# Optimization experiments

Hardware: AMD Instinct MI355X
Metric: run time of the kernel (lower is better)

## Reference

```python
import jax, jax.numpy as jnp
import numpy as np

HID = 64
L = 3
RHO = 0.3
KMIN = 64
EPS = 1e-5


def conv1x1(x, w, b):
    # x: [B,C,H,W], w: [O,C], b: [O]
    return jnp.einsum('bchw,oc->bohw', x, w) + b[None, :, None, None]


def dwconv(x, w, pad, dil):
    # depthwise conv, w: [C,1,k,k], groups = C, no bias
    return jax.lax.conv_general_dilated(
        x, w, window_strides=(1, 1), padding=[(pad, pad), (pad, pad)],
        rhs_dilation=(dil, dil), feature_group_count=x.shape[1],
        dimension_numbers=('NCHW', 'OIHW', 'NCHW'))


def conv3x3(x, w, b):
    return jax.lax.conv_general_dilated(
        x, w, (1, 1), [(1, 1), (1, 1)],
        dimension_numbers=('NCHW', 'OIHW', 'NCHW')) + b[None, :, None, None]


def bn(x, g, b):
    # training-mode BatchNorm2d: batch statistics over (B,H,W) per channel
    mu = jnp.mean(x, axis=(0, 2, 3), keepdims=True)
    var = jnp.var(x, axis=(0, 2, 3), keepdims=True)
    return g[None, :, None, None] * (x - mu) * jax.lax.rsqrt(var + EPS) + b[None, :, None, None]


def setup_inputs() -> dict:
    key = jax.random.key(0)
    ks = jax.random.split(key, 40)
    B, C, H, W = 8, 1, 224, 224
    d = {}
    d['x'] = jax.random.normal(ks[0], (B, C, H, W), jnp.float32)
    # input_proj: 1x1 conv, out = 2*HID + L + 1 = 132
    d['w_in'] = jax.random.normal(ks[1], (2 * HID + L + 1, C), jnp.float32) * 0.5
    d['b_in'] = jnp.zeros((2 * HID + L + 1,), jnp.float32)
    for l in range(L):
        ksz = 2 * l + 3
        d[f'dw{l}'] = jax.random.normal(ks[2 + 4 * l], (HID, 1, ksz, ksz), jnp.float32) / ksz
        d[f'pw{l}_w'] = jax.random.normal(ks[3 + 4 * l], (HID, HID), jnp.float32) * (1.0 / np.sqrt(HID))
        d[f'pw{l}_b'] = jnp.zeros((HID,), jnp.float32)
        d[f'bn{l}_g'] = jnp.ones((HID,), jnp.float32)
        d[f'bn{l}_b'] = jnp.zeros((HID,), jnp.float32)
    d['imp_w1'] = jax.random.normal(ks[20], (HID // 4, HID), jnp.float32) * (1.0 / np.sqrt(HID))
    d['imp_b1'] = jnp.zeros((HID // 4,), jnp.float32)
    d['imp_w2'] = jax.random.normal(ks[21], (1, HID // 4, 3, 3), jnp.float32) * 0.1
    d['imp_b2'] = jnp.zeros((1,), jnp.float32)
    d['val_w'] = jax.random.normal(ks[22], (HID, HID), jnp.float32) * (1.0 / np.sqrt(HID))
    d['val_b'] = jnp.zeros((HID,), jnp.float32)
    d['out_w'] = jax.random.normal(ks[23], (HID, HID), jnp.float32) * (1.0 / np.sqrt(HID))
    d['out_b'] = jnp.zeros((HID,), jnp.float32)
    d['fin_w'] = jax.random.normal(ks[24], (HID, HID), jnp.float32) * (1.0 / np.sqrt(HID))
    d['fin_b'] = jnp.zeros((HID,), jnp.float32)
    return d


def reference(x, w_in, b_in,
              dw0, pw0_w, pw0_b, bn0_g, bn0_b,
              dw1, pw1_w, pw1_b, bn1_g, bn1_b,
              dw2, pw2_w, pw2_b, bn2_g, bn2_b,
              imp_w1, imp_b1, imp_w2, imp_b2,
              val_w, val_b, out_w, out_b, fin_w, fin_b):
    B, C, H, W = x.shape
    F_ = conv1x1(x, w_in, b_in)                       # [B, 2*HID+L+1, H, W]
    Q = F_[:, :HID]
    K = F_[:, HID:2 * HID]
    G = F_[:, 2 * HID:]                               # [B, L+1, H, W]
    # importance network: 1x1 conv -> ReLU -> 3x3 conv -> sigmoid
    imp = jax.nn.sigmoid(conv3x3(jax.nn.relu(conv1x1(K, imp_w1, imp_b1)), imp_w2, imp_b2))  # [B,1,H,W]
    # adaptive top-k sparsification: K = max(floor(rho*H*W), K_min)
    k = max(int(RHO * H * W), KMIN)
    mask_flat = imp.reshape(B, H * W)
    _, idx = jax.lax.top_k(mask_flat, k)              # [B, k]
    sparse = jnp.zeros_like(mask_flat).at[jnp.arange(B)[:, None], idx].set(1.0)
    K_cur = K * sparse.reshape(B, 1, H, W)
    # focal levels: kernel k_l = 2*l+3, dilation d_l = 2^l, pad = (k_l//2)*d_l
    levels = [(dw0, pw0_w, pw0_b, bn0_g, bn0_b, 1),
              (dw1, pw1_w, pw1_b, bn1_g, bn1_b, 2),
              (dw2, pw2_w, pw2_b, bn2_g, bn2_b, 4)]
    focal = []
    for dw, pw_w, pw_b, g, be, dil in levels:
        ksz = dw.shape[-1]
        pad = (ksz // 2) * dil
        K_cur = jax.nn.relu(bn(conv1x1(dwconv(K_cur, dw, pad, dil), pw_w, pw_b), g, be))
        focal.append(K_cur)
    Gn = jax.nn.softmax(G, axis=1)                    # softmax over L+1 gate channels
    K_agg = Gn[:, 0:1] * focal[0] + Gn[:, 1:2] * focal[1] + Gn[:, 2:3] * focal[2]
    K_global = jnp.mean(focal[-1], axis=(2, 3), keepdims=True)  # AdaptiveAvgPool2d(1), broadcast
    K_final = K_agg + Gn[:, -1:] * K_global
    V = conv1x1(K_final, val_w, val_b)
    QV = Q * V
    # output_proj Linear over channel dim (dropout is identity in eval)
    O = jnp.einsum('bchw,oc->bohw', QV, out_w) + out_b[None, :, None, None]
    # in_channels (1) != hidden_channels -> residual via final_conv on F[:, :HID] == Q
    x_proj = conv1x1(Q, fin_w, fin_b)
    return x_proj + O
```

## Files before the change

### kernel.cpp

```cpp
#include <hip/hip_runtime.h>

#define HDIM 224
#define WDIM 224
#define PPIX 50176
#define BATCH 8
#define NPIX 401408
#define KTOP 15052
#define NELEM 25690112
#define NBLK 6272
#define NBAND 14
#define NDWBLK 7168
#define NCHUNK 49

typedef __attribute__((ext_vector_type(8))) short bf8_t;
typedef __attribute__((ext_vector_type(4))) float f4_t;
typedef __attribute__((ext_vector_type(8))) unsigned short us8_t;
typedef __attribute__((ext_vector_type(4))) unsigned short us4_t;
#define MFMA_BF16 __builtin_amdgcn_mfma_f32_16x16x32_bf16

__device__ inline unsigned short f2bf(float f) {
    unsigned int u = __float_as_uint(f);
    return (unsigned short)((u + 0x7FFFu + ((u >> 16) & 1u)) >> 16);
}
__device__ inline float bf2f(unsigned short u) {
    return __uint_as_float(((unsigned int)u) << 16);
}

__device__ inline int ldsg(int r) { return ((r >> 3) ^ r) & 7; }

__device__ inline void stage_w64(const float* __restrict__ W, char* sWc, int t) {
    int o = t >> 2, cq = t & 3, c0 = cq * 16;
    const float4* src = (const float4*)(W + o * 64 + c0);
    float4 v0 = src[0], v1 = src[1], v2 = src[2], v3 = src[3];
    bf8_t p0, p1;
    p0[0] = (short)f2bf(v0.x); p0[1] = (short)f2bf(v0.y);
    p0[2] = (short)f2bf(v0.z); p0[3] = (short)f2bf(v0.w);
    p0[4] = (short)f2bf(v1.x); p0[5] = (short)f2bf(v1.y);
    p0[6] = (short)f2bf(v1.z); p0[7] = (short)f2bf(v1.w);
    p1[0] = (short)f2bf(v2.x); p1[1] = (short)f2bf(v2.y);
    p1[2] = (short)f2bf(v2.z); p1[3] = (short)f2bf(v2.w);
    p1[4] = (short)f2bf(v3.x); p1[5] = (short)f2bf(v3.y);
    p1[6] = (short)f2bf(v3.z); p1[7] = (short)f2bf(v3.w);
    int g = ldsg(o);
    *(bf8_t*)(sWc + o * 128 + (((2 * cq) ^ g) << 4)) = p0;
    *(bf8_t*)(sWc + o * 128 + (((2 * cq + 1) ^ g) << 4)) = p1;
}

__device__ inline void mfma64(const char* sWc, const char* sPc, int l, int m0, f4_t acc[4]) {
    int lr = l & 15, lg = l >> 4;
    int ra = m0 + lr, ga = ldsg(ra);
    const char* abase = sWc + ra * 128;
    bf8_t a0 = *(const bf8_t*)(abase + ((lg ^ ga) << 4));
    bf8_t a1 = *(const bf8_t*)(abase + (((lg + 4) ^ ga) << 4));
    #pragma unroll
    for (int nt = 0; nt < 4; nt++) {
        int rb = nt * 16 + lr, gb = ldsg(rb);
        const char* bbase = sPc + rb * 128;
        bf8_t b0 = *(const bf8_t*)(bbase + ((lg ^ gb) << 4));
        bf8_t b1 = *(const bf8_t*)(bbase + (((lg + 4) ^ gb) << 4));
        f4_t c = {0.f, 0.f, 0.f, 0.f};
        c = MFMA_BF16(a0, b0, c, 0, 0, 0);
        c = MFMA_BF16(a1, b1, c, 0, 0, 0);
        acc[nt] = c;
    }
}

__global__ __launch_bounds__(256) void prep_kernel(
    const float* __restrict__ w_in, const float* __restrict__ b_in,
    const float* __restrict__ imp_w1, const float* __restrict__ imp_b1,
    const float* __restrict__ fin_w, const float* __restrict__ fin_b,
    float* __restrict__ coeffs, unsigned int* __restrict__ ghist,
    unsigned int* __restrict__ pfx, int* __restrict__ rem)
{
    int t = threadIdx.x;
    if (t < 16) {
        float a = 0.f, d = 0.f;
        for (int c = 0; c < 64; c++) {
            a += imp_w1[t * 64 + c] * w_in[64 + c];
            d += imp_w1[t * 64 + c] * b_in[64 + c];
        }
        coeffs[t] = a;
        coeffs[16 + t] = d + imp_b1[t];
    }
    if (t < 64) {
        float a = 0.f, d = 0.f;
        for (int c = 0; c < 64; c++) {
            a += fin_w[t * 64 + c] * w_in[c];
            d += fin_w[t * 64 + c] * b_in[c];
        }
        coeffs[32 + t] = a;
        coeffs[96 + t] = d + fin_b[t];
    }
    for (int i = t; i < 2048; i += 256) ghist[i] = 0u;
    if (t < BATCH) { pfx[t] = 0u; rem[t] = KTOP; }
}

__global__ __launch_bounds__(256) void imp_kernel(
    const float* __restrict__ x, const float* __restrict__ coeffs,
    const float* __restrict__ imp_w2, const float* __restrict__ imp_b2,
    float* __restrict__ imp)
{
    int idx = blockIdx.x * 256 + threadIdx.x;
    int b = idx / PPIX, p = idx % PPIX;
    int h = p / WDIM, w = p % WDIM;
    float acc = imp_b2[0];
    #pragma unroll
    for (int ky = 0; ky < 3; ky++) {
        int hh = h + ky - 1;
        float okh = (hh >= 0 && hh < HDIM) ? 1.f : 0.f;
        int hc = min(max(hh, 0), HDIM - 1);
        #pragma unroll
        for (int kx = 0; kx < 3; kx++) {
            int ww = w + kx - 1;
            float ok = okh * ((ww >= 0 && ww < WDIM) ? 1.f : 0.f);
            int wc = min(max(ww, 0), WDIM - 1);
            float xv = x[b * PPIX + hc * WDIM + wc] * ok;
            #pragma unroll
            for (int c = 0; c < 16; c++) {
                float r = fmaxf(xv * coeffs[c] + coeffs[16 + c] * ok, 0.f);
                acc += r * imp_w2[c * 9 + ky * 3 + kx];
            }
        }
    }
    imp[idx] = 1.f / (1.f + expf(-acc));
}

__global__ __launch_bounds__(256) void topk_hist(
    const float* __restrict__ imp, const unsigned int* __restrict__ pfx,
    unsigned int* __restrict__ ghist, int shift)
{
    int b = blockIdx.x / NCHUNK, ch = blockIdx.x % NCHUNK;
    int t = threadIdx.x;
    __shared__ unsigned int hist[256];
    hist[t] = 0u;
    __syncthreads();
    unsigned int prefix = pfx[b];
    unsigned int himask = (shift == 24) ? 0u : (0xFFFFFFFFu << (shift + 8));
    float4 v = ((const float4*)(imp + b * PPIX + ch * 1024))[t];
    unsigned int bb[4] = {__float_as_uint(v.x), __float_as_uint(v.y),
                          __float_as_uint(v.z), __float_as_uint(v.w)};
    #pragma unroll
    for (int k = 0; k < 4; k++)
        if ((bb[k] & himask) == prefix)
            atomicAdd(&hist[(bb[k] >> shift) & 255u], 1u);
    __syncthreads();
    unsigned int c = hist[t];
    if (c) atomicAdd(&ghist[b * 256 + t], c);
}

__global__ __launch_bounds__(256) void topk_select(
    unsigned int* __restrict__ ghist, unsigned int* __restrict__ pfx,
    int* __restrict__ rem, int shift)
{
    int b = blockIdx.x;
    int t = threadIdx.x;
    __shared__ unsigned int h[256];
    h[t] = ghist[b * 256 + t];
    ghist[b * 256 + t] = 0u;
    __syncthreads();
    if (t == 0) {
        int r = rem[b];
        unsigned int bsel = 0u;
        for (int bin = 255; bin >= 0; bin--) {
            int c = (int)h[bin];
            if (c >= r) { bsel = (unsigned int)bin; break; }
            r -= c;
        }
        rem[b] = r;
        pfx[b] |= bsel << shift;
    }
}

__global__ __launch_bounds__(256) void topk_mask1(
    const float* __restrict__ imp, const unsigned int* __restrict__ pfx,
    float* __restrict__ mask, int* __restrict__ blocktie)
{
    int b = blockIdx.x / NCHUNK, ch = blockIdx.x % NCHUNK;
    int t = threadIdx.x;
    unsigned int T = pfx[b];
    float4 v = ((const float4*)(imp + b * PPIX + ch * 1024))[t];
    unsigned int bb[4] = {__float_as_uint(v.x), __float_as_uint(v.y),
                          __float_as_uint(v.z), __float_as_uint(v.w)};
    float4 mo;
    float* mp = &mo.x;
    int cnt = 0;
    #pragma unroll
    for (int k = 0; k < 4; k++) {
        mp[k] = (bb[k] > T) ? 1.f : 0.f;
        cnt += (bb[k] == T) ? 1 : 0;
    }
    ((float4*)(mask + b * PPIX + ch * 1024))[t] = mo;
    #pragma unroll
    for (int off = 32; off > 0; off >>= 1) cnt += __shfl_down(cnt, off);
    __shared__ int ws4[4];
    int lane = t & 63, wv = t >> 6;
    if (lane == 0) ws4[wv] = cnt;
    __syncthreads();
    if (t == 0) blocktie[b * NCHUNK + ch] = ws4[0] + ws4[1] + ws4[2] + ws4[3];
}

__global__ __launch_bounds__(256) void topk_mask2(
    const float* __restrict__ imp, const unsigned int* __restrict__ pfx,
    const int* __restrict__ rem_, const int* __restrict__ blocktie,
    float* __restrict__ mask)
{
    int b = blockIdx.x;
    int t = threadIdx.x, lane = t & 63, wv = t >> 6;
    unsigned int T = pfx[b];
    int rem = rem_[b];
    __shared__ int sbase[NCHUNK], scnt[NCHUNK];
    if (t == 0) {
        int s = 0;
        for (int i = 0; i < NCHUNK; i++) {
            sbase[i] = s;
            int c = blocktie[b * NCHUNK + i];
            scnt[i] = c;
            s += c;
        }
    }
    __syncthreads();
    __shared__ int wtot[4];
    for (int ch = 0; ch < NCHUNK; ch++) {
        if (scnt[ch] == 0) continue;
        int base = sbase[ch];
        if (base >= rem) break;
        for (int g = 0; g < 4; g++) {
            int i = b * PPIX + ch * 1024 + g * 256 + t;
            int flag = (__float_as_uint(imp[i]) == T) ? 1 : 0;
            unsigned long long bal = __ballot(flag);
            if (lane == 0) wtot[wv] = __popcll(bal);
            __syncthreads();
            int wbase = 0, tot = 0;
            for (int q = 0; q < 4; q++) { int c = wtot[q]; if (q < wv) wbase += c; tot += c; }
            if (flag && base + wbase + __popcll(bal & ((1ull << lane) - 1ull)) < rem)
                mask[i] = 1.f;
            base += tot;
            __syncthreads();
        }
    }
}

__global__ __launch_bounds__(256, 4) void level0_kernel(
    const float* __restrict__ x, const float* __restrict__ mask,
    const float* __restrict__ w_in, const float* __restrict__ b_in,
    const float* __restrict__ dw_w, const float* __restrict__ pw_w,
    const float* __restrict__ pw_b,
    unsigned short* __restrict__ y_out, float* __restrict__ partials)
{
    __shared__ __align__(16) short sW[4096];
    __shared__ __align__(16) short sP[4096];
    __shared__ float sred[128];
    __shared__ float sBias[64];
    char* sWc = (char*)sW; char* sPc = (char*)sP;
    int t = threadIdx.x;
    int swz = (blockIdx.x & 7) * 784 + (blockIdx.x >> 3);
    int b = swz / 784;
    int l = t & 63, og = t >> 6;
    int p0 = (swz % 784) * 64;
    int p = p0 + l;
    int h = p / WDIM, w = p % WDIM;
    stage_w64(pw_w, sWc, t);
    if (t < 64) sBias[t] = pw_b[t];

    int rowoff[3]; float okhf[3];
    int wcs[3]; float okwf[3];
    #pragma unroll
    for (int k = 0; k < 3; k++) {
        int hh = h + k - 1;
        okhf[k] = (hh >= 0 && hh < HDIM) ? 1.f : 0.f;
        rowoff[k] = min(max(hh, 0), HDIM - 1) * WDIM;
        int ww = w + k - 1;
        okwf[k] = (ww >= 0 && ww < WDIM) ? 1.f : 0.f;
        wcs[k] = min(max(ww, 0), WDIM - 1);
    }
    float mv[9], mxv[9];
    const float* mb = mask + b * PPIX;
    const float* xb = x + b * PPIX;
    #pragma unroll
    for (int ky = 0; ky < 3; ky++) {
        #pragma unroll
        for (int kx = 0; kx < 3; kx++) {
            int a = rowoff[ky] + wcs[kx];
            float mm = mb[a] * (okhf[ky] * okwf[kx]);
            mv[ky * 3 + kx] = mm;
            mxv[ky * 3 + kx] = mm * xb[a];
        }
    }
    bf8_t pk0, pk1;
    #pragma unroll
    for (int j = 0; j < 16; j++) {
        int c = og * 16 + j;
        float wk = w_in[64 + c], bk = b_in[64 + c];
        const float* dwr = dw_w + c * 9;
        float a0 = 0.f, a1 = 0.f;
        #pragma unroll
        for (int tp = 0; tp < 9; tp++) {
            float dv = dwr[tp];
            a0 += dv * mxv[tp];
            a1 += dv * mv[tp];
        }
        unsigned short bv = f2bf(wk * a0 + bk * a1);
        if (j < 8) pk0[j] = (short)bv; else pk1[j - 8] = (short)bv;
    }
    int gl = ldsg(l);
    *(bf8_t*)(sPc + l * 128 + (((2 * og) ^ gl) << 4)) = pk0;
    *(bf8_t*)(sPc + l * 128 + (((2 * og + 1) ^ gl) << 4)) = pk1;
    __syncthreads();

    int m0 = og * 16, lr = l & 15, lg = l >> 4;
    f4_t acc[4];
    mfma64(sWc, sPc, l, m0, acc);
    unsigned short* ybase = y_out + (size_t)b * 64 * PPIX + p0;
    #pragma unroll
    for (int r = 0; r < 4; r++) {
        int o = m0 + 4 * lg + r;
        float bias = sBias[o];
        float s = 0.f, s2 = 0.f;
        #pragma unroll
        for (int nt = 0; nt < 4; nt++) {
            float yv = acc[nt][r] + bias;
            ybase[(size_t)o * PPIX + nt * 16 + lr] = f2bf(yv);
            s += yv; s2 += yv * yv;
        }
        #pragma unroll
        for (int m = 1; m < 16; m <<= 1) {
            s += __shfl_xor(s, m);
            s2 += __shfl_xor(s2, m);
        }
        if (lr == 0) { sred[2 * o] = s; sred[2 * o + 1] = s2; }
    }
    __syncthreads();
    if (t < 128) partials[(size_t)blockIdx.x * 128 + t] = sred[t];
}

template<int KSZ, int DIL>
__global__ __launch_bounds__(256, 4) void dw_kernel(
    const unsigned short* __restrict__ in, const float* __restrict__ bnp,
    const float* __restrict__ dw_w, unsigned short* __restrict__ out)
{
    constexpr int PAD = (KSZ / 2) * DIL;
    constexpr int BH = 16;
    constexpr int LR = BH + 2 * PAD;
    constexpr int SW = WDIM + 2 * PAD + 4;
    constexpr int SEG = 16 + 2 * PAD;
    __shared__ float sIn[LR * SW];

    int t = threadIdx.x;
    int swz = (blockIdx.x & 7) * (NDWBLK / 8) + (blockIdx.x >> 3);
    int bc = swz / NBAND, band = swz % NBAND;
    int c = bc & 63;
    int r0 = band * BH;
    float sc = bnp[c], sh = bnp[64 + c];
    const unsigned short* plane = in + (size_t)bc * PPIX;

    constexpr int PADC = SW - WDIM;
    for (int i = t; i < LR * PADC; i += 256) {
        int r = i / PADC, cc = i % PADC;
        int col = (cc < PAD) ? cc : (cc + WDIM);
        sIn[r * SW + col] = 0.f;
    }
    for (int i = t; i < LR * 28; i += 256) {
        int sr = i / 28, q = i % 28;
        int gr = r0 - PAD + sr;
        float4 a = {0.f, 0.f, 0.f, 0.f}, bq = {0.f, 0.f, 0.f, 0.f};
        if (gr >= 0 && gr < HDIM) {
            us8_t v = *(const us8_t*)(plane + gr * WDIM + 8 * q);
            a.x = fmaxf(sc * bf2f(v[0]) + sh, 0.f);
            a.y = fmaxf(sc * bf2f(v[1]) + sh, 0.f);
            a.z = fmaxf(sc * bf2f(v[2]) + sh, 0.f);
            a.w = fmaxf(sc * bf2f(v[3]) + sh, 0.f);
            bq.x = fmaxf(sc * bf2f(v[4]) + sh, 0.f);
            bq.y = fmaxf(sc * bf2f(v[5]) + sh, 0.f);
            bq.z = fmaxf(sc * bf2f(v[6]) + sh, 0.f);
            bq.w = fmaxf(sc * bf2f(v[7]) + sh, 0.f);
        }
        *(float4*)(sIn + sr * SW + PAD + 8 * q) = a;
        *(float4*)(sIn + sr * SW + PAD + 8 * q + 4) = bq;
    }
    __syncthreads();

    if (t < 224) {
        const float* dwr = dw_w + c * KSZ * KSZ;
        float wk[KSZ * KSZ];
        #pragma unroll
        for (int i = 0; i < KSZ * KSZ; i++) wk[i] = dwr[i];

        int row = t & 15, xs = t >> 4;
        int x0 = xs * 16;
        float acc[16];
        #pragma unroll
        for (int j = 0; j < 16; j++) acc[j] = 0.f;
        #pragma unroll
        for (int ky = 0; ky < KSZ; ky++) {
            const float4* srow = (const float4*)(sIn + (row + ky * DIL) * SW + x0);
            float s[SEG];
            #pragma unroll
            for (int i = 0; i < SEG / 4; i++) ((float4*)s)[i] = srow[i];
            #pragma unroll
            for (int kx = 0; kx < KSZ; kx++) {
                float wv = wk[ky * KSZ + kx];
                #pragma unroll
                for (int j = 0; j < 16; j++)
                    acc[j] += s[j + DIL * kx] * wv;
            }
        }
        us8_t o0, o1;
        #pragma unroll
        for (int j = 0; j < 8; j++) { o0[j] = f2bf(acc[j]); o1[j] = f2bf(acc[8 + j]); }
        unsigned short* orow = out + (size_t)bc * PPIX + (r0 + row) * WDIM + x0;
        *(us8_t*)orow = o0;
        *(us8_t*)(orow + 8) = o1;
    }
}

__global__ __launch_bounds__(256, 4) void pw_kernel(
    const float* __restrict__ pw_w, const float* __restrict__ pw_b,
    const unsigned short* __restrict__ src_y, unsigned short* __restrict__ dst_y,
    float* __restrict__ partials)
{
    __shared__ __align__(16) short sW[4096];
    __shared__ __align__(16) short sP[4096];
    __shared__ float sred[128];
    __shared__ float sBias[64];
    char* sWc = (char*)sW; char* sPc = (char*)sP;
    int t = threadIdx.x;
    int swz = (blockIdx.x & 7) * 784 + (blockIdx.x >> 3);
    int b = swz / 784;
    int p0 = (swz % 784) * 64;
    stage_w64(pw_w, sWc, t);
    if (t < 64) sBias[t] = pw_b[t];

    const unsigned short* sbase_g = src_y + (size_t)b * 64 * PPIX + p0;
    unsigned short* dbase_g = dst_y + (size_t)b * 64 * PPIX + p0;
    {
        int c = t >> 2, pg = t & 3;
        const unsigned short* src = sbase_g + (size_t)c * PPIX + 16 * pg;
        us8_t v0 = *(const us8_t*)src;
        us8_t v1 = *(const us8_t*)(src + 8);
        int kc = c >> 3, cb = 2 * (c & 7);
        #pragma unroll
        for (int e = 0; e < 16; e++) {
            int r = 16 * pg + e;
            int gr = ldsg(r);
            unsigned short val = (e < 8) ? (unsigned short)v0[e] : (unsigned short)v1[e - 8];
            *(unsigned short*)(sPc + r * 128 + ((kc ^ gr) << 4) + cb) = val;
        }
    }
    __syncthreads();

    int l = t & 63, wv = t >> 6, m0 = wv * 16;
    int lr = l & 15, lg = l >> 4;
    f4_t acc[4];
    mfma64(sWc, sPc, l, m0, acc);
    #pragma unroll
    for (int r = 0; r < 4; r++) {
        int o = m0 + 4 * lg + r;
        float bias = sBias[o];
        float s = 0.f, s2 = 0.f;
        #pragma unroll
        for (int nt = 0; nt < 4; nt++) {
            float yv = acc[nt][r] + bias;
            dbase_g[(size_t)o * PPIX + nt * 16 + lr] = f2bf(yv);
            s += yv; s2 += yv * yv;
        }
        #pragma unroll
        for (int m = 1; m < 16; m <<= 1) {
            s += __shfl_xor(s, m);
            s2 += __shfl_xor(s2, m);
        }
        if (lr == 0) { sred[2 * o] = s; sred[2 * o + 1] = s2; }
    }
    __syncthreads();
    if (t < 128) partials[(size_t)blockIdx.x * 128 + t] = sred[t];
}

__global__ __launch_bounds__(256) void bnfin_kernel(
    const float* __restrict__ partials,
    const float* __restrict__ g, const float* __restrict__ be,
    float* __restrict__ bnp)
{
    int c = blockIdx.x;
    int t = threadIdx.x;
    float s = 0.f, s2 = 0.f;
    for (int blk = t; blk < NBLK; blk += 256) {
        s  += partials[(size_t)blk * 128 + 2 * c];
        s2 += partials[(size_t)blk * 128 + 2 * c + 1];
    }
    #pragma unroll
    for (int off = 32; off > 0; off >>= 1) {
        s += __shfl_down(s, off);
        s2 += __shfl_down(s2, off);
    }
    __shared__ float wsm[8];
    int lane = t & 63, wv = t >> 6;
    if (lane == 0) { wsm[wv] = s; wsm[4 + wv] = s2; }
    __syncthreads();
    if (t == 0) {
        s = wsm[0] + wsm[1] + wsm[2] + wsm[3];
        s2 = wsm[4] + wsm[5] + wsm[6] + wsm[7];
        const float inv_n = 1.f / (float)NPIX;
        float mu = s * inv_n;
        float var = s2 * inv_n - mu * mu;
        float sc = g[c] * rsqrtf(var + 1e-5f);
        bnp[c] = sc;
        bnp[64 + c] = be[c] - mu * sc;
    }
}

__global__ __launch_bounds__(1024) void kglobal_kernel(
    const unsigned short* __restrict__ y2, const float* __restrict__ bnp2,
    float* __restrict__ kg)
{
    int bc = blockIdx.x;
    int c = bc & 63;
    int t = threadIdx.x;
    const unsigned short* row = y2 + (size_t)bc * PPIX;
    float sc = bnp2[c], sh = bnp2[64 + c];
    float s = 0.f;
    for (int ii = t; ii < PPIX / 8; ii += 1024) {
        us8_t v = *(const us8_t*)(row + 8 * ii);
        #pragma unroll
        for (int k = 0; k < 8; k++) s += fmaxf(sc * bf2f(v[k]) + sh, 0.f);
    }
    #pragma unroll
    for (int off = 32; off > 0; off >>= 1) s += __shfl_down(s, off);
    __shared__ float wsum[16];
    int lane = t & 63, wv = t >> 6;
    if (lane == 0) wsum[wv] = s;
    __syncthreads();
    if (t == 0) {
        float tot = 0.f;
        #pragma unroll
        for (int q = 0; q < 16; q++) tot += wsum[q];
        kg[bc] = tot * (1.f / (float)PPIX);
    }
}

__global__ __launch_bounds__(256, 4) void final_kernel(
    const float* __restrict__ x, const float* __restrict__ w_in,
    const float* __restrict__ b_in,
    const unsigned short* __restrict__ y0, const unsigned short* __restrict__ y1,
    const unsigned short* __restrict__ y2,
    const float* __restrict__ bnp, const float* __restrict__ kg,
    const float* __restrict__ val_w, const float* __restrict__ val_b,
    const float* __restrict__ out_w, const float* __restrict__ out_b,
    const float* __restrict__ coeffs, float* __restrict__ out)
{
    __shared__ __align__(16) short sVW[4096];
    __shared__ __align__(16) short sOW[4096];
    __shared__ __align__(16) short sP[4096];
    __shared__ float sxv[64], sG[320];
    __shared__ float sQW[64], sQB[64], sVB[64], sOB[64], sC1[64], sC2[64];
    char* sVWc = (char*)sVW; char* sOWc = (char*)sOW; char* sPc = (char*)sP;
    int t = threadIdx.x;
    int blk = blockIdx.x;
    int b = blk / 784;
    int l = t & 63, wv = t >> 6;
    int p0 = (blk % 784) * 64;
    stage_w64(val_w, sVWc, t);
    stage_w64(out_w, sOWc, t);
    if (t < 64) {
        sQW[t] = w_in[t]; sQB[t] = b_in[t];
        sVB[t] = val_b[t]; sOB[t] = out_b[t];
        sC1[t] = coeffs[32 + t]; sC2[t] = coeffs[96 + t];
        float xv = x[b * PPIX + p0 + t];
        sxv[t] = xv;
        float g0 = xv * w_in[128] + b_in[128];
        float g1 = xv * w_in[129] + b_in[129];
        float g2 = xv * w_in[130] + b_in[130];
        float g3 = xv * w_in[131] + b_in[131];
        float mx = fmaxf(fmaxf(g0, g1), fmaxf(g2, g3));
        float e0 = expf(g0 - mx), e1 = expf(g1 - mx);
        float e2 = expf(g2 - mx), e3 = expf(g3 - mx);
        float inv = 1.f / (e0 + e1 + e2 + e3);
        sG[5 * t + 0] = e0 * inv;
        sG[5 * t + 1] = e1 * inv;
        sG[5 * t + 2] = e2 * inv;
        sG[5 * t + 3] = e3 * inv;
    }
    __syncthreads();

    {
        int c = t >> 2, pg = t & 3;
        size_t base = (size_t)(b * 64 + c) * PPIX + p0 + 16 * pg;
        us8_t a0 = *(const us8_t*)(y0 + base);
        us8_t a1 = *(const us8_t*)(y0 + base + 8);
        us8_t q0 = *(const us8_t*)(y1 + base);
        us8_t q1 = *(const us8_t*)(y1 + base + 8);
        us8_t r0 = *(const us8_t*)(y2 + base);
        us8_t r1 = *(const us8_t*)(y2 + base + 8);
        float s0 = bnp[c],       h0 = bnp[64 + c];
        float s1 = bnp[128 + c], h1 = bnp[192 + c];
        float s2 = bnp[256 + c], h2 = bnp[320 + c];
        float kgc = kg[b * 64 + c];
        int kc = c >> 3, cb = 2 * (c & 7);
        #pragma unroll
        for (int e = 0; e < 16; e++) {
            unsigned short u0 = (e < 8) ? (unsigned short)a0[e] : (unsigned short)a1[e - 8];
            unsigned short u1 = (e < 8) ? (unsigned short)q0[e] : (unsigned short)q1[e - 8];
            unsigned short u2 = (e < 8) ? (unsigned short)r0[e] : (unsigned short)r1[e - 8];
            float f0 = fmaxf(s0 * bf2f(u0) + h0, 0.f);
            float f1 = fmaxf(s1 * bf2f(u1) + h1, 0.f);
            float f2 = fmaxf(s2 * bf2f(u2) + h2, 0.f);
            int r = 16 * pg + e;
            float kf = sG[5 * r] * f0 + sG[5 * r + 1] * f1
                     + sG[5 * r + 2] * f2 + sG[5 * r + 3] * kgc;
            int gr = ldsg(r);
            *(unsigned short*)(sPc + r * 128 + ((kc ^ gr) << 4) + cb) = f2bf(kf);
        }
    }
    __syncthreads();

    int m0 = wv * 16, lr = l & 15, lg = l >> 4;
    f4_t accV[4];
    mfma64(sVWc, sPc, l, m0, accV);
    __syncthreads();

    #pragma unroll
    for (int nt = 0; nt < 4; nt++) {
        float xvp = sxv[nt * 16 + lr];
        us4_t q4;
        #pragma unroll
        for (int r = 0; r < 4; r++) {
            int o = m0 + 4 * lg + r;
            float V = accV[nt][r] + sVB[o];
            float q = xvp * sQW[o] + sQB[o];
            q4[r] = f2bf(q * V);
        }
        int rb = nt * 16 + lr, gb = ldsg(rb);
        int kc = 2 * wv + (lg >> 1);
        *(us4_t*)(sPc + rb * 128 + ((kc ^ gb) << 4) + 8 * (lg & 1)) = q4;
    }
    __syncthreads();

    f4_t accO[4];
    mfma64(sOWc, sPc, l, m0, accO);
    #pragma unroll
    for (int nt = 0; nt < 4; nt++) {
        float xvp = sxv[nt * 16 + lr];
        #pragma unroll
        for (int r = 0; r < 4; r++) {
            int o = m0 + 4 * lg + r;
            out[(size_t)(b * 64 + o) * PPIX + p0 + nt * 16 + lr] =
                accO[nt][r] + sOB[o] + xvp * sC1[o] + sC2[o];
        }
    }
}

extern "C" void kernel_launch(void* const* d_in, const int* in_sizes, int n_in,
                              void* d_out, int out_size, void* d_ws, size_t ws_size,
                              hipStream_t stream)
{
    (void)in_sizes; (void)n_in; (void)out_size; (void)ws_size;
    const float* x      = (const float*)d_in[0];
    const float* w_in   = (const float*)d_in[1];
    const float* b_in   = (const float*)d_in[2];
    const float* dw0    = (const float*)d_in[3];
    const float* pw0_w  = (const float*)d_in[4];
    const float* pw0_b  = (const float*)d_in[5];
    const float* bn0_g  = (const float*)d_in[6];
    const float* bn0_b  = (const float*)d_in[7];
    const float* dw1    = (const float*)d_in[8];
    const float* pw1_w  = (const float*)d_in[9];
    const float* pw1_b  = (const float*)d_in[10];
    const float* bn1_g  = (const float*)d_in[11];
    const float* bn1_b  = (const float*)d_in[12];
    const float* dw2    = (const float*)d_in[13];
    const float* pw2_w  = (const float*)d_in[14];
    const float* pw2_b  = (const float*)d_in[15];
    const float* bn2_g  = (const float*)d_in[16];
    const float* bn2_b  = (const float*)d_in[17];
    const float* imp_w1 = (const float*)d_in[18];
    const float* imp_b1 = (const float*)d_in[19];
    const float* imp_w2 = (const float*)d_in[20];
    const float* imp_b2 = (const float*)d_in[21];
    const float* val_w  = (const float*)d_in[22];
    const float* val_b  = (const float*)d_in[23];
    const float* out_w  = (const float*)d_in[24];
    const float* out_b  = (const float*)d_in[25];
    const float* fin_w  = (const float*)d_in[26];
    const float* fin_b  = (const float*)d_in[27];

    unsigned short* y0 = (unsigned short*)d_ws;
    unsigned short* y1 = y0 + (size_t)NELEM;
    unsigned short* y2 = y1 + (size_t)NELEM;
    unsigned short* yt = y2 + (size_t)NELEM;
    float* imp  = (float*)(yt + (size_t)NELEM);
    float* mask = imp + NPIX;
    float* partials = mask + NPIX;
    float* bnp   = partials + (size_t)NBLK * 128;
    float* kg    = bnp + 384;
    float* coeffs = kg + 512;
    unsigned int* ghist = (unsigned int*)(coeffs + 160);
    unsigned int* pfx   = ghist + 2048;
    int* rem            = (int*)(pfx + 8);
    int* blocktie       = rem + 8;
    float* outp = (float*)d_out;

    prep_kernel<<<1, 256, 0, stream>>>(w_in, b_in, imp_w1, imp_b1, fin_w, fin_b,
                                       coeffs, ghist, pfx, rem);
    imp_kernel<<<NPIX / 256, 256, 0, stream>>>(x, coeffs, imp_w2, imp_b2, imp);

    for (int shift = 24; shift >= 0; shift -= 8) {
        topk_hist<<<BATCH * NCHUNK, 256, 0, stream>>>(imp, pfx, ghist, shift);
        topk_select<<<BATCH, 256, 0, stream>>>(ghist, pfx, rem, shift);
    }
    topk_mask1<<<BATCH * NCHUNK, 256, 0, stream>>>(imp, pfx, mask, blocktie);
    topk_mask2<<<BATCH, 256, 0, stream>>>(imp, pfx, rem, blocktie, mask);

    level0_kernel<<<NBLK, 256, 0, stream>>>(x, mask, w_in, b_in, dw0, pw0_w, pw0_b,
                                            y0, partials);
    bnfin_kernel<<<64, 256, 0, stream>>>(partials, bn0_g, bn0_b, bnp);

    dw_kernel<5, 2><<<NDWBLK, 256, 0, stream>>>(y0, bnp, dw1, yt);
    pw_kernel<<<NBLK, 256, 0, stream>>>(pw1_w, pw1_b, yt, y1, partials);
    bnfin_kernel<<<64, 256, 0, stream>>>(partials, bn1_g, bn1_b, bnp + 128);

    dw_kernel<7, 4><<<NDWBLK, 256, 0, stream>>>(y1, bnp + 128, dw2, yt);
    pw_kernel<<<NBLK, 256, 0, stream>>>(pw2_w, pw2_b, yt, y2, partials);
    bnfin_kernel<<<64, 256, 0, stream>>>(partials, bn2_g, bn2_b, bnp + 256);

    kglobal_kernel<<<512, 1024, 0, stream>>>(y2, bnp + 256, kg);
    final_kernel<<<NBLK, 256, 0, stream>>>(x, w_in, b_in, y0, y1, y2, bnp, kg,
                                           val_w, val_b, out_w, out_b, coeffs, outp);
}
```

Measured before the change: 380.9 us.

## Compute two output rows per thread in depthwise conv to reuse loaded rows

The depthwise conv kernel now covers 32-row bands, and each thread computes two output rows spaced DIL apart. Because those two rows share all but one input row, each shared-memory row is loaded once and applied to both accumulators. This cuts LDS reads per output and halves the block count, with the halo overhead amortized over taller bands. In exchange it uses more shared memory and registers per block, and the 7x7 variant's occupancy bound is lowered to 2 blocks per CU.

```diff
diff --git a/kernel.cpp b/kernel.cpp
--- a/kernel.cpp
+++ b/kernel.cpp
@@ -8,8 +8,8 @@
 #define KTOP 15052
 #define NELEM 25690112
 #define NBLK 6272
-#define NBAND 14
-#define NDWBLK 7168
+#define NBAND2 7
+#define NDWBLK2 3584
 #define NCHUNK 49
 
 typedef __attribute__((ext_vector_type(8))) short bf8_t;
@@ -333,21 +333,21 @@
     if (t < 128) partials[(size_t)blockIdx.x * 128 + t] = sred[t];
 }
 
-template<int KSZ, int DIL>
-__global__ __launch_bounds__(256, 4) void dw_kernel(
+template<int KSZ, int DIL, int OCC>
+__global__ __launch_bounds__(256, OCC) void dw_kernel(
     const unsigned short* __restrict__ in, const float* __restrict__ bnp,
     const float* __restrict__ dw_w, unsigned short* __restrict__ out)
 {
     constexpr int PAD = (KSZ / 2) * DIL;
-    constexpr int BH = 16;
+    constexpr int BH = 32;
     constexpr int LR = BH + 2 * PAD;
     constexpr int SW = WDIM + 2 * PAD + 4;
     constexpr int SEG = 16 + 2 * PAD;
     __shared__ float sIn[LR * SW];
 
     int t = threadIdx.x;
-    int swz = (blockIdx.x & 7) * (NDWBLK / 8) + (blockIdx.x >> 3);
-    int bc = swz / NBAND, band = swz % NBAND;
+    int swz = (blockIdx.x & 7) * (NDWBLK2 / 8) + (blockIdx.x >> 3);
+    int bc = swz / NBAND2, band = swz % NBAND2;
     int c = bc & 63;
     int r0 = band * BH;
     float sc = bnp[c], sh = bnp[64 + c];
@@ -385,31 +385,49 @@
         #pragma unroll
         for (int i = 0; i < KSZ * KSZ; i++) wk[i] = dwr[i];
 
-        int row = t & 15, xs = t >> 4;
+        int pg = t & 15, xs = t >> 4;
+        int g = (pg % DIL) + 2 * DIL * (pg / DIL);
         int x0 = xs * 16;
-        float acc[16];
-        #pragma unroll
-        for (int j = 0; j < 16; j++) acc[j] = 0.f;
-        #pragma unroll
-        for (int ky = 0; ky < KSZ; ky++) {
-            const float4* srow = (const float4*)(sIn + (row + ky * DIL) * SW + x0);
-            float s[SEG];
+        float a0[16], a1[16];
+        #pragma unroll
+        for (int j = 0; j < 16; j++) { a0[j] = 0.f; a1[j] = 0.f; }
+        #pragma unroll
+        for (int s = 0; s <= KSZ; s++) {
+            const float4* srow = (const float4*)(sIn + (g + DIL * s) * SW + x0);
+            float sv[SEG];
             #pragma unroll
-            for (int i = 0; i < SEG / 4; i++) ((float4*)s)[i] = srow[i];
-            #pragma unroll
-            for (int kx = 0; kx < KSZ; kx++) {
-                float wv = wk[ky * KSZ + kx];
+            for (int i = 0; i < SEG / 4; i++) ((float4*)sv)[i] = srow[i];
+            if (s < KSZ) {
                 #pragma unroll
-                for (int j = 0; j < 16; j++)
-                    acc[j] += s[j + DIL * kx] * wv;
+                for (int kx = 0; kx < KSZ; kx++) {
+                    float wv = wk[s * KSZ + kx];
+                    #pragma unroll
+                    for (int j = 0; j < 16; j++)
+                        a0[j] += sv[j + DIL * kx] * wv;
+                }
             }
-        }
-        us8_t o0, o1;
-        #pragma unroll
-        for (int j = 0; j < 8; j++) { o0[j] = f2bf(acc[j]); o1[j] = f2bf(acc[8 + j]); }
-        unsigned short* orow = out + (size_t)bc * PPIX + (r0 + row) * WDIM + x0;
-        *(us8_t*)orow = o0;
-        *(us8_t*)(orow + 8) = o1;
+            if (s >= 1) {
+                #pragma unroll
+                for (int kx = 0; kx < KSZ; kx++) {
+                    float wv = wk[(s - 1) * KSZ + kx];
+                    #pragma unroll
+                    for (int j = 0; j < 16; j++)
+                        a1[j] += sv[j + DIL * kx] * wv;
+                }
+            }
+        }
+        us8_t o00, o01, o10, o11;
+        #pragma unroll
+        for (int j = 0; j < 8; j++) {
+            o00[j] = f2bf(a0[j]); o01[j] = f2bf(a0[8 + j]);
+            o10[j] = f2bf(a1[j]); o11[j] = f2bf(a1[8 + j]);
+        }
+        unsigned short* orow0 = out + (size_t)bc * PPIX + (r0 + g) * WDIM + x0;
+        unsigned short* orow1 = orow0 + DIL * WDIM;
+        *(us8_t*)orow0 = o00;
+        *(us8_t*)(orow0 + 8) = o01;
+        *(us8_t*)orow1 = o10;
+        *(us8_t*)(orow1 + 8) = o11;
     }
 }
 
@@ -712,11 +730,11 @@
                                             y0, partials);
     bnfin_kernel<<<64, 256, 0, stream>>>(partials, bn0_g, bn0_b, bnp);
 
-    dw_kernel<5, 2><<<NDWBLK, 256, 0, stream>>>(y0, bnp, dw1, yt);
+    dw_kernel<5, 2, 4><<<NDWBLK2, 256, 0, stream>>>(y0, bnp, dw1, yt);
     pw_kernel<<<NBLK, 256, 0, stream>>>(pw1_w, pw1_b, yt, y1, partials);
     bnfin_kernel<<<64, 256, 0, stream>>>(partials, bn1_g, bn1_b, bnp + 128);
 
-    dw_kernel<7, 4><<<NDWBLK, 256, 0, stream>>>(y1, bnp + 128, dw2, yt);
+    dw_kernel<7, 4, 2><<<NDWBLK2, 256, 0, stream>>>(y1, bnp + 128, dw2, yt);
     pw_kernel<<<NBLK, 256, 0, stream>>>(pw2_w, pw2_b, yt, y2, partials);
     bnfin_kernel<<<64, 256, 0, stream>>>(partials, bn2_g, bn2_b, bnp + 256);
 
```

Result: no change. 385.7 us (+1.3%).
